# Performance work log

Hardware: AMD Instinct MI355X
Metric: run time of the kernel (lower is better)

## Reference

```python
import jax, jax.numpy as jnp
import numpy as np

B, L, D, DFF, DLLM, E, TOPK = 16, 512, 768, 3072, 4096, 8, 2
EPS_GATE = 1e-9
LN_EPS = 1e-5


def _layernorm(x, gamma, beta):
    mu = jnp.mean(x, axis=-1, keepdims=True)
    var = jnp.var(x, axis=-1, keepdims=True)
    return (x - mu) * jax.lax.rsqrt(var + LN_EPS) * gamma + beta


def _mlp_block(x, w1, b1, w2, b2, gamma, beta):
    # MLPBlock: Linear -> GELU -> Linear -> LayerNorm(residual). Dropout is identity in eval.
    h = jax.nn.gelu(x @ w1 + b1)
    o = h @ w2 + b2
    return _layernorm(o + x, gamma, beta)


def setup_inputs() -> dict:
    key = jax.random.key(0)
    ks = jax.random.split(key, 24)
    sd = lambda fan_in: 1.0 / np.sqrt(fan_in)
    inp = {
        'cycle_curve_data': jax.random.normal(ks[0], (B, L, D), jnp.float32),
        'cycle_numbers': jax.random.uniform(ks[1], (B, 1), jnp.float32) * 1000.0,
        'DKP_embeddings': jax.random.normal(ks[2], (B, DLLM), jnp.float32),
        # Gate (PatternRouter_two): fuses LLM embedding + cycle number -> expert logits
        'gate_We': jax.random.normal(ks[3], (DLLM, DFF), jnp.float32) * sd(DLLM),
        'gate_Wc': jax.random.normal(ks[4], (1, DFF), jnp.float32),
        'gate_b': jnp.zeros((DFF,), jnp.float32),
        'gate_Wo': jax.random.normal(ks[5], (DFF, E), jnp.float32) * sd(DFF),
        'gate_bo': jnp.zeros((E,), jnp.float32),
        # Stacked expert params [E, ...]
        'e_w1': jax.random.normal(ks[6], (E, D, DFF), jnp.float32) * sd(D),
        'e_b1': jnp.zeros((E, DFF), jnp.float32),
        'e_w2': jax.random.normal(ks[7], (E, DFF, D), jnp.float32) * sd(DFF),
        'e_b2': jnp.zeros((E, D), jnp.float32),
        'e_gamma': jnp.ones((E, D), jnp.float32),
        'e_beta': jnp.zeros((E, D), jnp.float32),
        # General expert
        'g_w1': jax.random.normal(ks[8], (D, DFF), jnp.float32) * sd(D),
        'g_b1': jnp.zeros((DFF,), jnp.float32),
        'g_w2': jax.random.normal(ks[9], (DFF, D), jnp.float32) * sd(DFF),
        'g_b2': jnp.zeros((D,), jnp.float32),
        'g_gamma': jnp.ones((D,), jnp.float32),
        'g_beta': jnp.zeros((D,), jnp.float32),
    }
    return inp


def reference(cycle_curve_data, cycle_numbers, DKP_embeddings,
              gate_We, gate_Wc, gate_b, gate_Wo, gate_bo,
              e_w1, e_b1, e_w2, e_b2, e_gamma, e_beta,
              g_w1, g_b1, g_w2, g_b2, g_gamma, g_beta):
    # --- Router: clean logits (eval mode: no noise) ---
    h = jax.nn.relu(DKP_embeddings @ gate_We + cycle_numbers @ gate_Wc + gate_b)
    logits = h @ gate_Wo + gate_bo                         # [B, E]
    _, idx = jax.lax.top_k(logits, TOPK)                   # [B, TOPK]
    probs = jax.nn.softmax(logits, axis=1)
    mask = jnp.zeros_like(probs).at[jnp.arange(B)[:, None], idx].set(1.0)
    gated = probs * mask
    gated = gated / (jnp.sum(gated, axis=1, keepdims=True) + EPS_GATE)  # [B, E]

    # --- Experts: dense compute, zero gates zero out non-routed experts ---
    x = cycle_curve_data
    combined = jnp.zeros_like(x)
    for e in range(E):  # small fixed expert count
        out_e = _mlp_block(x, e_w1[e], e_b1[e], e_w2[e], e_b2[e], e_gamma[e], e_beta[e])
        combined = combined + gated[:, e, None, None] * out_e

    general = _mlp_block(x, g_w1, g_b1, g_w2, g_b2, g_gamma, g_beta)
    final_out = general + combined.astype(jnp.bfloat16)  # matches .to(torch.bfloat16) cast before add
    return final_out
```

## Files before the change

kernel.cpp:

```cpp
#include <hip/hip_runtime.h>
#include <cstdint>

#define B_    16
#define L_    512
#define D_    768
#define DFF_  3072
#define DLLM_ 4096
#define E_    8

typedef unsigned short ushort_t;
typedef __attribute__((ext_vector_type(4))) float accfrag_t;
typedef __attribute__((ext_vector_type(8))) short bfrag_t;

typedef __attribute__((address_space(3))) uint32_t lds_u32;
typedef __attribute__((address_space(1))) uint32_t glb_u32;

__device__ inline void gload16(const void* g, void* l) {
  __builtin_amdgcn_global_load_lds((const glb_u32*)(uintptr_t)g,
                                   (lds_u32*)(uint32_t)(uintptr_t)l, 16, 0, 0);
}

__device__ inline ushort_t f2bf(float f) {
  uint32_t u = __float_as_uint(f);
  return (ushort_t)((u + 0x7FFFu + ((u >> 16) & 1u)) >> 16);
}
__device__ inline float bf2f(ushort_t v) { return __uint_as_float(((uint32_t)v) << 16); }

#define MFMA16(a, b, c) __builtin_amdgcn_mfma_f32_16x16x32_bf16(a, b, c, 0, 0, 0)

template <int KT>
__device__ __forceinline__ void gemm_body(const char* gA, const char* gB,
                                          char* sm, accfrag_t acc[4][4]) {
  const int tid = threadIdx.x;
  const int lane = tid & 63;
  const int w = tid >> 6, wm = w >> 1, wn = w & 1;
  const int LDB = KT * 128;

  const int R0 = tid >> 3;
  const char* srcA = gA + (size_t)R0 * LDB + ((((tid & 7) ^ (R0 & 7)) << 4));
  const char* srcB = gB + (size_t)R0 * LDB + ((((tid & 7) ^ (R0 & 7)) << 4));
  const int dl = tid * 16;

  const int l15 = lane & 15, l7 = lane & 7, lhi = lane >> 4;
  const int a0 = (wm * 64 + l15) * 128 + ((lhi ^ l7) << 4);
  const int a1 = (wm * 64 + l15) * 128 + (((4 + lhi) ^ l7) << 4);
  const int b0 = 16384 + (wn * 64 + l15) * 128 + ((lhi ^ l7) << 4);
  const int b1 = 16384 + (wn * 64 + l15) * 128 + (((4 + lhi) ^ l7) << 4);

#pragma unroll 1
  for (int t = 0; t < KT; ++t) {
    const size_t ko = (size_t)t * 128;
#pragma unroll
    for (int j = 0; j < 4; ++j)
      gload16(srcA + (size_t)j * 32 * LDB + ko, sm + j * 4096 + dl);
#pragma unroll
    for (int j = 0; j < 4; ++j)
      gload16(srcB + (size_t)j * 32 * LDB + ko, sm + 16384 + j * 4096 + dl);
    __syncthreads();
    bfrag_t af0[4], af1[4], bf0[4], bf1[4];
#pragma unroll
    for (int nf = 0; nf < 4; ++nf) {
      bf0[nf] = *(const bfrag_t*)(sm + b0 + nf * 2048);
      bf1[nf] = *(const bfrag_t*)(sm + b1 + nf * 2048);
    }
#pragma unroll
    for (int mf = 0; mf < 4; ++mf) {
      af0[mf] = *(const bfrag_t*)(sm + a0 + mf * 2048);
      af1[mf] = *(const bfrag_t*)(sm + a1 + mf * 2048);
    }
    __builtin_amdgcn_s_setprio(1);
#pragma unroll
    for (int mf = 0; mf < 4; ++mf)
#pragma unroll
      for (int nf = 0; nf < 4; ++nf) {
        acc[mf][nf] = MFMA16(af0[mf], bf0[nf], acc[mf][nf]);
        acc[mf][nf] = MFMA16(af1[mf], bf1[nf], acc[mf][nf]);
      }
    __builtin_amdgcn_s_setprio(0);
    __syncthreads();
  }
}

__global__ __launch_bounds__(256, 3)
void gemm1_k(const ushort_t* __restrict__ xb, const ushort_t* __restrict__ w1t,
             const float* __restrict__ e_b1, const float* __restrict__ g_b1,
             const int* __restrict__ tidx, ushort_t* __restrict__ h_out, int job0) {
  __shared__ char sm[32768];
  const int bx = blockIdx.x;
  const int mt = bx & 3, nt = bx >> 2;
  const int jp = blockIdx.y, job = job0 + jp;
  const int b = job / 3, s = job - b * 3;
  const int e = (s < 2) ? tidx[b * 2 + s] : E_;
  const char* gA = (const char*)(xb + ((size_t)b * L_ + mt * 128) * D_);
  const char* gB = (const char*)(w1t + ((size_t)e * DFF_ + nt * 128) * D_);
  accfrag_t acc[4][4] = {};
  gemm_body<12>(gA, gB, sm, acc);

  const float* b1 = (s < 2) ? (e_b1 + (size_t)e * DFF_) : g_b1;
  const int tid = threadIdx.x, lane = tid & 63, w = tid >> 6;
  const int wm = w >> 1, wn = w & 1;
#pragma unroll
  for (int nf = 0; nf < 4; ++nf) {
    const int col = wn * 64 + nf * 16 + (lane & 15);
    const float bias = b1[nt * 128 + col];
#pragma unroll
    for (int mf = 0; mf < 4; ++mf)
#pragma unroll
      for (int r = 0; r < 4; ++r) {
        const int row = wm * 64 + mf * 16 + ((lane >> 4) << 2) + r;
        float v = acc[mf][nf][r] + bias;
        float u = 0.7978845608028654f * (v + 0.044715f * v * v * v);
        float th = 1.0f - 2.0f / (1.0f + __expf(2.0f * u));
        const int phys = (col >> 3) ^ (row & 7);
        *(ushort_t*)(sm + row * 256 + phys * 16 + (col & 7) * 2) =
            f2bf(0.5f * v * (1.0f + th));
      }
  }
  __syncthreads();
  ushort_t* hbase = h_out + ((size_t)jp * L_ + mt * 128) * DFF_ + nt * 128;
#pragma unroll
  for (int i = 0; i < 8; ++i) {
    const int g = tid + i * 256;
    const int row = g >> 4, c16 = g & 15;
    const uint4 v = *(const uint4*)(sm + row * 256 + (c16 ^ (row & 7)) * 16);
    *(uint4*)((char*)(hbase + (size_t)row * DFF_) + c16 * 16) = v;
  }
}

__global__ __launch_bounds__(256, 3)
void gemm2_k(const ushort_t* __restrict__ h_in, const ushort_t* __restrict__ w2t,
             const float* __restrict__ e_b2, const float* __restrict__ g_b2,
             const float* __restrict__ x_f, const int* __restrict__ tidx,
             ushort_t* __restrict__ slot_o, float* __restrict__ outp, int job0) {
  __shared__ char sm[32768];
  const int bx = blockIdx.x;
  const int mt = bx & 3, nt = bx >> 2;
  const int jp = blockIdx.y, job = job0 + jp;
  const int b = job / 3, s = job - b * 3;
  const int e = (s < 2) ? tidx[b * 2 + s] : E_;
  const char* gA = (const char*)(h_in + ((size_t)jp * L_ + mt * 128) * DFF_);
  const char* gB = (const char*)(w2t + ((size_t)e * D_ + nt * 128) * DFF_);
  accfrag_t acc[4][4] = {};
  gemm_body<48>(gA, gB, sm, acc);

  const float* b2 = (s < 2) ? (e_b2 + (size_t)e * D_) : g_b2;
  const int lane = threadIdx.x & 63, w = threadIdx.x >> 6;
  const int wm = w >> 1, wn = w & 1;
  const int row0 = mt * 128 + wm * 64 + ((lane >> 4) << 2);
  const int col0 = nt * 128 + wn * 64 + (lane & 15);
#pragma unroll
  for (int mf = 0; mf < 4; ++mf)
#pragma unroll
    for (int nf = 0; nf < 4; ++nf) {
      const int col = col0 + nf * 16;
      const float bias = b2[col];
#pragma unroll
      for (int r = 0; r < 4; ++r) {
        const int row = row0 + mf * 16 + r;
        float v = acc[mf][nf][r] + bias + x_f[((size_t)b * L_ + row) * D_ + col];
        if (s < 2)
          slot_o[(((size_t)b * 2 + s) * L_ + row) * D_ + col] = f2bf(v);
        else
          outp[((size_t)b * L_ + row) * D_ + col] = v;
      }
    }
}

__global__ __launch_bounds__(256)
void transpose_cvt_k(const float* __restrict__ srcE, const float* __restrict__ srcG,
                     ushort_t* __restrict__ dst, int R, int C) {
  const int z = blockIdx.z;
  const float* src = (z < 8) ? (srcE + (size_t)z * R * C) : srcG;
  ushort_t* out = dst + (size_t)z * R * C;
  __shared__ float tile[64][65];
  const int c0 = blockIdx.x * 64, r0 = blockIdx.y * 64;
  const int t = threadIdx.x;
  const int rr = t >> 4, cc = (t & 15) * 4;
#pragma unroll
  for (int i = 0; i < 4; ++i) {
    const float4 v = *(const float4*)(src + (size_t)(r0 + rr + i * 16) * C + c0 + cc);
    tile[rr + i * 16][cc] = v.x; tile[rr + i * 16][cc + 1] = v.y;
    tile[rr + i * 16][cc + 2] = v.z; tile[rr + i * 16][cc + 3] = v.w;
  }
  __syncthreads();
  const int c = t >> 2, r8 = (t & 3) * 16;
#pragma unroll
  for (int j = 0; j < 2; ++j) {
    ushort_t u[8];
#pragma unroll
    for (int k = 0; k < 8; ++k) u[k] = f2bf(tile[r8 + j * 8 + k][c]);
    *(uint4*)(out + (size_t)(c0 + c) * R + r0 + r8 + j * 8) = *(const uint4*)u;
  }
}

__global__ void cvt_x_k(const float* __restrict__ in, ushort_t* __restrict__ out) {
  const int i = (blockIdx.x * 256 + threadIdx.x) * 4;
  const float4 v = *(const float4*)(in + i);
  uint2 u;
  u.x = (uint32_t)f2bf(v.x) | ((uint32_t)f2bf(v.y) << 16);
  u.y = (uint32_t)f2bf(v.z) | ((uint32_t)f2bf(v.w) << 16);
  *(uint2*)(out + i) = u;
}

__global__ __launch_bounds__(256)
void router_partial_k(const float* __restrict__ emb, const float* __restrict__ We,
                      float* __restrict__ rp) {
  const int nt = blockIdx.x, kb = blockIdx.y;
  const int tid = threadIdx.x;
  __shared__ float semb[B_][256];
  const int k0 = kb * 256;
#pragma unroll
  for (int r = 0; r < B_; ++r) semb[r][tid] = emb[(size_t)r * DLLM_ + k0 + tid];
  __syncthreads();
  const int f = nt * 256 + tid;
  float acc[B_] = {};
  for (int k = 0; k < 256; ++k) {
    const float wv = We[(size_t)(k0 + k) * DFF_ + f];
#pragma unroll
    for (int j = 0; j < B_; ++j) acc[j] += semb[j][k] * wv;
  }
#pragma unroll
  for (int j = 0; j < B_; ++j)
    rp[((size_t)kb * B_ + j) * DFF_ + f] = acc[j];
}

__global__ void router_reduce_k(const float* __restrict__ rp, const float* __restrict__ cyc,
                                const float* __restrict__ Wc, const float* __restrict__ gb,
                                float* __restrict__ hr) {
  const int g = blockIdx.x * 256 + threadIdx.x;
  const int b = g / DFF_, f = g - b * DFF_;
  float s = 0.0f;
#pragma unroll
  for (int kb = 0; kb < 16; ++kb)
    s += rp[((size_t)kb * B_ + b) * DFF_ + f];
  s += cyc[b] * Wc[f] + gb[f];
  hr[(size_t)b * DFF_ + f] = fmaxf(s, 0.0f);
}

__global__ void router_final_k(const float* __restrict__ hr, const float* __restrict__ Wo,
                               const float* __restrict__ bo, int* __restrict__ tidx,
                               float* __restrict__ gates) {
  const int b = blockIdx.x, tid = threadIdx.x;
  float acc[E_] = {};
  for (int f = tid; f < DFF_; f += 256) {
    const float hv = hr[(size_t)b * DFF_ + f];
#pragma unroll
    for (int o = 0; o < E_; ++o) acc[o] += hv * Wo[(size_t)f * E_ + o];
  }
  __shared__ float lred[E_][4];
#pragma unroll
  for (int o = 0; o < E_; ++o) {
    float v = acc[o];
#pragma unroll
    for (int off = 32; off > 0; off >>= 1) v += __shfl_down(v, off, 64);
    if ((tid & 63) == 0) lred[o][tid >> 6] = v;
  }
  __syncthreads();
  if (tid == 0) {
    float lg[E_];
    float mx = -1e30f;
    for (int o = 0; o < E_; ++o) {
      lg[o] = lred[o][0] + lred[o][1] + lred[o][2] + lred[o][3] + bo[o];
      mx = fmaxf(mx, lg[o]);
    }
    int i1 = 0;
    for (int o = 1; o < E_; ++o) if (lg[o] > lg[i1]) i1 = o;
    int i2 = (i1 == 0) ? 1 : 0;
    for (int o = 0; o < E_; ++o) if (o != i1 && lg[o] > lg[i2]) i2 = o;
    float p[E_], sum = 0.0f;
    for (int o = 0; o < E_; ++o) { p[o] = __expf(lg[o] - mx); sum += p[o]; }
    const float p1 = p[i1] / sum, p2 = p[i2] / sum;
    const float den = p1 + p2 + 1e-9f;
    tidx[b * 2] = i1; tidx[b * 2 + 1] = i2;
    gates[b * 2] = p1 / den; gates[b * 2 + 1] = p2 / den;
  }
}

__global__ __launch_bounds__(256)
void final_ln_k(float* __restrict__ outp, const ushort_t* __restrict__ so,
                const float* __restrict__ gates, const int* __restrict__ tidx,
                const float* __restrict__ e_gam, const float* __restrict__ e_bet,
                const float* __restrict__ g_gam, const float* __restrict__ g_bet) {
  const int row = blockIdx.x;
  const int b = row >> 9, l = row & 511;
  const int tid = threadIdx.x;
  __shared__ float red4[4];
  float* gr = outp + (size_t)row * D_;
  const ushort_t* s0 = so + (((size_t)b * 2 + 0) * L_ + l) * D_;
  const ushort_t* s1 = so + (((size_t)b * 2 + 1) * L_ + l) * D_;
  float a0[3], a1[3], a2[3];
#pragma unroll
  for (int j = 0; j < 3; ++j) {
    const int d = tid + j * 256;
    a0[j] = gr[d];
    a1[j] = bf2f(s0[d]);
    a2[j] = bf2f(s1[d]);
  }
  auto bsum = [&](float v) -> float {
#pragma unroll
    for (int o = 32; o > 0; o >>= 1) v += __shfl_down(v, o, 64);
    if ((tid & 63) == 0) red4[tid >> 6] = v;
    __syncthreads();
    const float r = red4[0] + red4[1] + red4[2] + red4[3];
    __syncthreads();
    return r;
  };
  const float sg = bsum(a0[0] + a0[1] + a0[2]);
  const float qg = bsum(a0[0] * a0[0] + a0[1] * a0[1] + a0[2] * a0[2]);
  const float s0s = bsum(a1[0] + a1[1] + a1[2]);
  const float q0s = bsum(a1[0] * a1[0] + a1[1] * a1[1] + a1[2] * a1[2]);
  const float s1s = bsum(a2[0] + a2[1] + a2[2]);
  const float q1s = bsum(a2[0] * a2[0] + a2[1] * a2[1] + a2[2] * a2[2]);
  const float inv = 1.0f / 768.0f;
  const float mug = sg * inv, rg = rsqrtf(qg * inv - mug * mug + 1e-5f);
  const float mu0 = s0s * inv, r0 = rsqrtf(q0s * inv - mu0 * mu0 + 1e-5f);
  const float mu1 = s1s * inv, r1 = rsqrtf(q1s * inv - mu1 * mu1 + 1e-5f);
  const int e0 = tidx[b * 2], e1 = tidx[b * 2 + 1];
  const float g0 = gates[b * 2], g1 = gates[b * 2 + 1];
#pragma unroll
  for (int j = 0; j < 3; ++j) {
    const int d = tid + j * 256;
    const float lng = (a0[j] - mug) * rg * g_gam[d] + g_bet[d];
    const float ln0 = (a1[j] - mu0) * r0 * e_gam[(size_t)e0 * D_ + d] + e_bet[(size_t)e0 * D_ + d];
    const float ln1 = (a2[j] - mu1) * r1 * e_gam[(size_t)e1 * D_ + d] + e_bet[(size_t)e1 * D_ + d];
    const float comb = g0 * ln0 + g1 * ln1;
    gr[d] = lng + bf2f(f2bf(comb));
  }
}

extern "C" void kernel_launch(void* const* d_in, const int* in_sizes, int n_in,
                              void* d_out, int out_size, void* d_ws, size_t ws_size,
                              hipStream_t stream) {
  const float* x_f  = (const float*)d_in[0];
  const float* cyc  = (const float*)d_in[1];
  const float* emb  = (const float*)d_in[2];
  const float* We   = (const float*)d_in[3];
  const float* Wc   = (const float*)d_in[4];
  const float* gb   = (const float*)d_in[5];
  const float* Wo   = (const float*)d_in[6];
  const float* bo   = (const float*)d_in[7];
  const float* e_w1 = (const float*)d_in[8];
  const float* e_b1 = (const float*)d_in[9];
  const float* e_w2 = (const float*)d_in[10];
  const float* e_b2 = (const float*)d_in[11];
  const float* e_gam = (const float*)d_in[12];
  const float* e_bet = (const float*)d_in[13];
  const float* g_w1 = (const float*)d_in[14];
  const float* g_b1 = (const float*)d_in[15];
  const float* g_w2 = (const float*)d_in[16];
  const float* g_b2 = (const float*)d_in[17];
  const float* g_gam = (const float*)d_in[18];
  const float* g_bet = (const float*)d_in[19];
  float* outp = (float*)d_out;
  char* ws = (char*)d_ws;

  size_t off = 0;
  auto alloc = [&](size_t bytes) { size_t o = off; off = (off + bytes + 255) & ~(size_t)255; return o; };
  const size_t o_idx  = alloc(32 * 4);
  const size_t o_gate = alloc(32 * 4);
  const size_t o_hr   = alloc((size_t)B_ * DFF_ * 4);
  const size_t o_rp   = alloc((size_t)16 * B_ * DFF_ * 4);
  const size_t o_xb   = alloc((size_t)B_ * L_ * D_ * 2);
  const size_t o_w1t  = alloc((size_t)9 * DFF_ * D_ * 2);
  const size_t o_w2t  = alloc((size_t)9 * D_ * DFF_ * 2);
  const size_t o_so   = alloc((size_t)B_ * 2 * L_ * D_ * 2);
  const size_t o_h    = off;

  int JP = 1;
  const int divs[10] = {48, 24, 16, 12, 8, 6, 4, 3, 2, 1};
  for (int k = 0; k < 10; ++k) {
    if (o_h + (size_t)divs[k] * L_ * DFF_ * 2 <= ws_size) { JP = divs[k]; break; }
  }

  ushort_t* xb    = (ushort_t*)(ws + o_xb);
  ushort_t* w1t   = (ushort_t*)(ws + o_w1t);
  ushort_t* w2t   = (ushort_t*)(ws + o_w2t);
  ushort_t* so    = (ushort_t*)(ws + o_so);
  ushort_t* h_ws  = (ushort_t*)(ws + o_h);
  int*      tidx  = (int*)(ws + o_idx);
  float*    gates = (float*)(ws + o_gate);
  float*    hr    = (float*)(ws + o_hr);
  float*    rp    = (float*)(ws + o_rp);

  cvt_x_k<<<dim3((B_ * L_ * D_) / 1024), dim3(256), 0, stream>>>(x_f, xb);
  transpose_cvt_k<<<dim3(DFF_ / 64, D_ / 64, 9), dim3(256), 0, stream>>>(e_w1, g_w1, w1t, D_, DFF_);
  transpose_cvt_k<<<dim3(D_ / 64, DFF_ / 64, 9), dim3(256), 0, stream>>>(e_w2, g_w2, w2t, DFF_, D_);
  router_partial_k<<<dim3(12, 16), dim3(256), 0, stream>>>(emb, We, rp);
  router_reduce_k<<<dim3(192), dim3(256), 0, stream>>>(rp, cyc, Wc, gb, hr);
  router_final_k<<<dim3(16), dim3(256), 0, stream>>>(hr, Wo, bo, tidx, gates);

  const int passes = 48 / JP;
  for (int p = 0; p < passes; ++p) {
    gemm1_k<<<dim3(96, JP), dim3(256), 0, stream>>>(xb, w1t, e_b1, g_b1, tidx, h_ws, p * JP);
    gemm2_k<<<dim3(24, JP), dim3(256), 0, stream>>>(h_ws, w2t, e_b2, g_b2, x_f, tidx, so, outp, p * JP);
  }
  final_ln_k<<<dim3(B_ * L_), dim3(256), 0, stream>>>(outp, so, gates, tidx,
                                                      e_gam, e_bet, g_gam, g_bet);
}
```

Baseline: 485.7 us.

## Remap GEMM blocks per XCD by job and write GELU output directly

Both expert GEMM kernels switch to a 1D grid whose block index maps round-robin across the 8 XCDs. All tiles of one job then land on the same XCD, so that XCD's L2 can share the job's weight and activation tiles. Tile order inside a job also changes to M-major. The gemm1 epilogue drops the LDS-staged, swizzled 16-byte coalesced store in favour of direct 2-byte scattered global stores, which removes a barrier but risks poorer write coalescing. Bias loads are also hoisted out of the inner loops.

Measured after the change: 474.5 us. 1.02x faster.

```diff
diff --git a/kernel.cpp b/kernel.cpp
--- a/kernel.cpp
+++ b/kernel.cpp
@@ -81,14 +81,28 @@
   }
 }
 
+__device__ inline void job_tile(int f, int tilesPerJob, int jp_count,
+                                int& jobIdx, int& t) {
+  if ((jp_count & 7) == 0) {
+    const int xcd = f & 7, slot = f >> 3;
+    jobIdx = xcd + 8 * (slot / tilesPerJob);
+    t = slot % tilesPerJob;
+  } else {
+    jobIdx = f / tilesPerJob;
+    t = f % tilesPerJob;
+  }
+}
+
 __global__ __launch_bounds__(256, 3)
 void gemm1_k(const ushort_t* __restrict__ xb, const ushort_t* __restrict__ w1t,
              const float* __restrict__ e_b1, const float* __restrict__ g_b1,
-             const int* __restrict__ tidx, ushort_t* __restrict__ h_out, int job0) {
+             const int* __restrict__ tidx, ushort_t* __restrict__ h_out,
+             int job0, int jp_count) {
   __shared__ char sm[32768];
-  const int bx = blockIdx.x;
-  const int mt = bx & 3, nt = bx >> 2;
-  const int jp = blockIdx.y, job = job0 + jp;
+  int jp, t;
+  job_tile(blockIdx.x, 96, jp_count, jp, t);
+  const int mt = t / 24, nt = t % 24;
+  const int job = job0 + jp;
   const int b = job / 3, s = job - b * 3;
   const int e = (s < 2) ? tidx[b * 2 + s] : E_;
   const char* gA = (const char*)(xb + ((size_t)b * L_ + mt * 128) * D_);
@@ -97,45 +111,40 @@
   gemm_body<12>(gA, gB, sm, acc);
 
   const float* b1 = (s < 2) ? (e_b1 + (size_t)e * DFF_) : g_b1;
-  const int tid = threadIdx.x, lane = tid & 63, w = tid >> 6;
+  const int lane = threadIdx.x & 63, w = threadIdx.x >> 6;
   const int wm = w >> 1, wn = w & 1;
-#pragma unroll
-  for (int nf = 0; nf < 4; ++nf) {
-    const int col = wn * 64 + nf * 16 + (lane & 15);
-    const float bias = b1[nt * 128 + col];
-#pragma unroll
-    for (int mf = 0; mf < 4; ++mf)
-#pragma unroll
-      for (int r = 0; r < 4; ++r) {
-        const int row = wm * 64 + mf * 16 + ((lane >> 4) << 2) + r;
-        float v = acc[mf][nf][r] + bias;
+  const int row0 = mt * 128 + wm * 64 + ((lane >> 4) << 2);
+  const int col0 = nt * 128 + wn * 64 + (lane & 15);
+  float bias[4];
+#pragma unroll
+  for (int nf = 0; nf < 4; ++nf) bias[nf] = b1[col0 + nf * 16];
+  ushort_t* hp = h_out + (size_t)jp * L_ * DFF_ + (size_t)row0 * DFF_ + col0;
+#pragma unroll
+  for (int mf = 0; mf < 4; ++mf)
+#pragma unroll
+    for (int r = 0; r < 4; ++r) {
+      ushort_t* hr_ = hp + (size_t)(mf * 16 + r) * DFF_;
+#pragma unroll
+      for (int nf = 0; nf < 4; ++nf) {
+        float v = acc[mf][nf][r] + bias[nf];
         float u = 0.7978845608028654f * (v + 0.044715f * v * v * v);
         float th = 1.0f - 2.0f / (1.0f + __expf(2.0f * u));
-        const int phys = (col >> 3) ^ (row & 7);
-        *(ushort_t*)(sm + row * 256 + phys * 16 + (col & 7) * 2) =
-            f2bf(0.5f * v * (1.0f + th));
+        hr_[nf * 16] = f2bf(0.5f * v * (1.0f + th));
       }
-  }
-  __syncthreads();
-  ushort_t* hbase = h_out + ((size_t)jp * L_ + mt * 128) * DFF_ + nt * 128;
-#pragma unroll
-  for (int i = 0; i < 8; ++i) {
-    const int g = tid + i * 256;
-    const int row = g >> 4, c16 = g & 15;
-    const uint4 v = *(const uint4*)(sm + row * 256 + (c16 ^ (row & 7)) * 16);
-    *(uint4*)((char*)(hbase + (size_t)row * DFF_) + c16 * 16) = v;
-  }
+    }
 }
 
 __global__ __launch_bounds__(256, 3)
 void gemm2_k(const ushort_t* __restrict__ h_in, const ushort_t* __restrict__ w2t,
              const float* __restrict__ e_b2, const float* __restrict__ g_b2,
              const float* __restrict__ x_f, const int* __restrict__ tidx,
-             ushort_t* __restrict__ slot_o, float* __restrict__ outp, int job0) {
+             ushort_t* __restrict__ slot_o, float* __restrict__ outp,
+             int job0, int jp_count) {
   __shared__ char sm[32768];
-  const int bx = blockIdx.x;
-  const int mt = bx & 3, nt = bx >> 2;
-  const int jp = blockIdx.y, job = job0 + jp;
+  int jp, t;
+  job_tile(blockIdx.x, 24, jp_count, jp, t);
+  const int mt = t / 6, nt = t % 6;
+  const int job = job0 + jp;
   const int b = job / 3, s = job - b * 3;
   const int e = (s < 2) ? tidx[b * 2 + s] : E_;
   const char* gA = (const char*)(h_in + ((size_t)jp * L_ + mt * 128) * DFF_);
@@ -148,20 +157,22 @@
   const int wm = w >> 1, wn = w & 1;
   const int row0 = mt * 128 + wm * 64 + ((lane >> 4) << 2);
   const int col0 = nt * 128 + wn * 64 + (lane & 15);
+  float bias[4];
+#pragma unroll
+  for (int nf = 0; nf < 4; ++nf) bias[nf] = b2[col0 + nf * 16];
 #pragma unroll
   for (int mf = 0; mf < 4; ++mf)
 #pragma unroll
-    for (int nf = 0; nf < 4; ++nf) {
-      const int col = col0 + nf * 16;
-      const float bias = b2[col];
-#pragma unroll
-      for (int r = 0; r < 4; ++r) {
-        const int row = row0 + mf * 16 + r;
-        float v = acc[mf][nf][r] + bias + x_f[((size_t)b * L_ + row) * D_ + col];
+    for (int r = 0; r < 4; ++r) {
+      const int row = row0 + mf * 16 + r;
+      const float* xr = x_f + ((size_t)b * L_ + row) * D_ + col0;
+#pragma unroll
+      for (int nf = 0; nf < 4; ++nf) {
+        float v = acc[mf][nf][r] + bias[nf] + xr[nf * 16];
         if (s < 2)
-          slot_o[(((size_t)b * 2 + s) * L_ + row) * D_ + col] = f2bf(v);
+          slot_o[(((size_t)b * 2 + s) * L_ + row) * D_ + col0 + nf * 16] = f2bf(v);
         else
-          outp[((size_t)b * L_ + row) * D_ + col] = v;
+          outp[((size_t)b * L_ + row) * D_ + col0 + nf * 16] = v;
       }
     }
 }
@@ -391,8 +402,8 @@
 
   const int passes = 48 / JP;
   for (int p = 0; p < passes; ++p) {
-    gemm1_k<<<dim3(96, JP), dim3(256), 0, stream>>>(xb, w1t, e_b1, g_b1, tidx, h_ws, p * JP);
-    gemm2_k<<<dim3(24, JP), dim3(256), 0, stream>>>(h_ws, w2t, e_b2, g_b2, x_f, tidx, so, outp, p * JP);
+    gemm1_k<<<dim3(96 * JP), dim3(256), 0, stream>>>(xb, w1t, e_b1, g_b1, tidx, h_ws, p * JP, JP);
+    gemm2_k<<<dim3(24 * JP), dim3(256), 0, stream>>>(h_ws, w2t, e_b2, g_b2, x_f, tidx, so, outp, p * JP, JP);
   }
   final_ln_k<<<dim3(B_ * L_), dim3(256), 0, stream>>>(outp, so, gates, tidx,
                                                       e_gam, e_bet, g_gam, g_bet);
```
